# Kernel tuning notes

Measured on AMD Instinct MI355X. Metric: run time of the kernel, lower is better.

The kernel has to match this reference:

```python
import jax, jax.numpy as jnp
import numpy as np

SHIFT, REDUCE = 0, 1
B, T, E, H, V, O = 128, 256, 300, 256, 32000, 5


def _rand_trans(rng, n_tok):
    # valid shift-reduce sequence: n_tok SHIFTs, n_tok-1 REDUCEs
    seq = np.empty(2 * n_tok - 1, np.int32)
    shifts = 0
    depth = 0
    for i in range(2 * n_tok - 1):
        if shifts < n_tok and (depth < 2 or rng.random() < 0.6):
            seq[i] = SHIFT; shifts += 1; depth += 1
        else:
            seq[i] = REDUCE; depth -= 1
    return seq


def setup_inputs() -> dict:
    key = jax.random.key(0)
    ks = jax.random.split(key, 10)
    rng = np.random.default_rng(0)
    x_ids = jax.random.randint(ks[0], (B, T), 0, V)
    transitions = jnp.asarray(np.stack([_rand_trans(rng, T) for _ in range(B)], axis=1))  # [2T-1, B]
    u = lambda k, shape, s: jax.random.uniform(k, shape, jnp.float32, -s, s)
    sE = 1.0 / np.sqrt(E)
    sH = 1.0 / np.sqrt(H)
    embed_table = (jax.random.normal(ks[1], (V, E), jnp.float32) * 0.1).at[1].set(0.0)  # padding_idx=1
    return dict(
        x_ids=x_ids, transitions=transitions, embed_table=embed_table,
        Wp=u(ks[2], (H, E), sE), bp=u(ks[3], (H,), sE),
        Wg=u(ks[4], (H, E), sE), bg=u(ks[5], (H,), sE),
        Wr=u(ks[6], (5 * H, 2 * H), sH), br=u(ks[7], (5 * H,), sH),
        Wo=u(ks[8], (O, H), sH), bo=u(ks[9], (O,), sH),
    )


def reference(x_ids, transitions, embed_table, Wp, bp, Wg, bg, Wr, br, Wo, bo):
    Hh = Wp.shape[0]
    Bn, Tn = x_ids.shape
    emb = embed_table[x_ids]                                   # [B,T,E]
    c_buf = jnp.einsum('bte,he->bth', emb, Wp) + bp            # proj_x
    h_buf = jnp.tanh(c_buf) * jax.nn.sigmoid(jnp.einsum('bte,he->bth', emb, Wg) + bg)
    buffers = jnp.concatenate([h_buf, c_buf], axis=-1)         # [B,T,2H]
    bidx = jnp.arange(Bn)

    def cell(left, right):
        hl, cl = jnp.split(left, 2, axis=-1)
        hr, cr = jnp.split(right, 2, axis=-1)
        proj = jnp.concatenate([hl, hr], axis=-1) @ Wr.T + br  # [B,5H]
        i, fl, fr, g, o = jnp.split(proj, 5, axis=-1)
        c_new = jax.nn.sigmoid(i) * jnp.tanh(g) + jax.nn.sigmoid(fl) * cl + jax.nn.sigmoid(fr) * cr
        h_new = jax.nn.sigmoid(o) * jnp.tanh(c_new)
        return jnp.concatenate([h_new, c_new], axis=-1)

    def step(carry, t_batch):
        stack, sptr, bptr = carry
        is_shift = (t_batch == SHIFT)
        shifted = buffers[bidx, bptr - 1]                      # buffer.pop() = last token first
        left = stack[bidx, sptr - 2]
        right = stack[bidx, sptr - 1]
        reduced = cell(left, right)
        new_state = jnp.where(is_shift[:, None], shifted, reduced)
        new_sptr = jnp.where(is_shift, sptr + 1, sptr - 1)
        new_bptr = jnp.where(is_shift, bptr - 1, bptr)
        stack = stack.at[bidx, new_sptr - 1].set(new_state)    # push (shift or reduce result)
        return (stack, new_sptr, new_bptr), None

    init = (jnp.zeros((Bn, Tn, 2 * Hh), buffers.dtype),
            jnp.zeros((Bn,), jnp.int32), jnp.full((Bn,), Tn, jnp.int32))
    (stack, sptr, _), _ = jax.lax.scan(step, init, transitions)
    final_h = stack[bidx, sptr - 1][:, :Hh]                    # root h
    logits = final_h @ Wo.T + bo                               # dropout is identity in eval
    return logits
```

## Files before the change

### kernel.cpp

```cpp
#include <hip/hip_runtime.h>
#include <hip/hip_bf16.h>

#define B 128
#define T 256
#define E 300
#define HH 256
#define O 5
#define NSTEP (2*T - 1)
#define NINT 255
#define NG 8
#define PSTR 41
#define LMAX_DIRECT 176
#define BAR_STRIDE 16
#define BAR_WORDS ((32 + 2) * BAR_STRIDE)

__device__ __forceinline__ float sigm(float x) { return 1.f / (1.f + __expf(-x)); }

__device__ __forceinline__ void grid_barrier(unsigned* bar, int myN) {
  __syncthreads();
  if (threadIdx.x == 0) {
    __threadfence();
    const int per_sub = (int)(gridDim.x >> 5);
    const int s = (int)(blockIdx.x & 31);
    unsigned r = atomicAdd(&bar[s * BAR_STRIDE], 1u);
    if (r == (unsigned)(myN * per_sub - 1)) {
      unsigned q = atomicAdd(&bar[32 * BAR_STRIDE], 1u);
      if (q == (unsigned)(myN * 32 - 1)) {
        atomicAdd(&bar[33 * BAR_STRIDE], 1u);
      }
    }
    while (__hip_atomic_load(&bar[33 * BAR_STRIDE], __ATOMIC_ACQUIRE,
                             __HIP_MEMORY_SCOPE_AGENT) < (unsigned)myN) {
      __builtin_amdgcn_s_sleep(2);
    }
    __threadfence();
  }
  __syncthreads();
}

__global__ __launch_bounds__(256) void k_transpose(
    const float* __restrict__ Wp, const float* __restrict__ Wg,
    const float* __restrict__ Wr, float* __restrict__ WcT,
    float* __restrict__ W4) {
  int idx = blockIdx.x * 256 + threadIdx.x;
  if (idx < HH * E) {
    int h = idx / E;
    int e = idx % E;
    WcT[e * 512 + h]       = Wp[idx];
    WcT[e * 512 + 256 + h] = Wg[idx];
  }
  if (idx < 5 * HH * 2 * HH) {
    int j = idx / 512;
    int k = idx % 512;
    W4[((size_t)(k >> 2) * 1280 + j) * 4 + (k & 3)] = Wr[idx];
  }
}

#define TT 16
__global__ __launch_bounds__(256) void k_buffers(
    const int* __restrict__ x_ids, const float* __restrict__ embed,
    const float* __restrict__ WcT, const float* __restrict__ bp,
    const float* __restrict__ bg, float* __restrict__ buffers) {
  __shared__ float lds[TT * E];
  const int b  = blockIdx.y;
  const int t0 = blockIdx.x * TT;
  const int tid = threadIdx.x;

  for (int i = tid; i < TT * E; i += 256) {
    int t = i / E;
    int e = i % E;
    int id = x_ids[b * T + t0 + t];
    lds[i] = embed[(size_t)id * E + e];
  }
  __syncthreads();

  const int h = tid;
  float accP[TT], accG[TT];
#pragma unroll
  for (int t = 0; t < TT; ++t) { accP[t] = bp[h]; accG[t] = bg[h]; }

  for (int e = 0; e < E; ++e) {
    float wp = WcT[e * 512 + h];
    float wg = WcT[e * 512 + 256 + h];
#pragma unroll
    for (int t = 0; t < TT; ++t) {
      float x = lds[t * E + e];
      accP[t] = fmaf(x, wp, accP[t]);
      accG[t] = fmaf(x, wg, accG[t]);
    }
  }

#pragma unroll
  for (int t = 0; t < TT; ++t) {
    float c  = accP[t];
    float hb = tanhf(c) * sigm(accG[t]);
    size_t base = ((size_t)b * T + t0 + t) * 512;
    buffers[base + h]       = hb;
    buffers[base + 256 + h] = c;
  }
}

__global__ __launch_bounds__(128) void k_prep(
    const int* __restrict__ trans, int* __restrict__ meta,
    int* __restrict__ levCnt, int* __restrict__ levOff, int* __restrict__ maxLevG,
    int* __restrict__ rootA, unsigned* __restrict__ worklist,
    unsigned short* __restrict__ stkG, unsigned* __restrict__ bar) {
  __shared__ int cnt[256];
  __shared__ int off[256];
  __shared__ int cur[256];
  const int b = threadIdx.x;
  for (int i = b; i < 256; i += 128) cnt[i] = 0;
  for (int i = b; i < BAR_WORDS; i += 128) bar[i] = 0u;
  __syncthreads();

  int sp = 0, bp = T, r = 0;
  for (int s = 0; s < NSTEP; ++s) {
    int tr = trans[s * B + b];
    if (tr == 0) {
      stkG[sp * 128 + b] = (unsigned short)(bp - 1);
      sp++; bp--;
    } else {
      int idR = stkG[(sp - 1) * 128 + b];
      int idL = stkG[(sp - 2) * 128 + b];
      sp -= 2;
      int lL = (idL < 256) ? 0 : (meta[b * NINT + idL - 256] >> 18);
      int lR = (idR < 256) ? 0 : (meta[b * NINT + idR - 256] >> 18);
      int lev = max(lL, lR) + 1;
      meta[b * NINT + r] = idL | (idR << 9) | (lev << 18);
      atomicAdd(&cnt[lev], 1);
      stkG[sp * 128 + b] = (unsigned short)(256 + r);
      sp++; r++;
    }
  }
  rootA[b] = (int)stkG[0 * 128 + b];
  __syncthreads();

  if (b == 0) {
    int acc = 0, ml = 1;
    for (int l = 0; l < 256; ++l) {
      off[l] = acc; acc += cnt[l];
      if (cnt[l] > 0) ml = l;
    }
    *maxLevG = ml;
  }
  __syncthreads();
  for (int i = b; i < 256; i += 128) { levCnt[i] = cnt[i]; levOff[i] = off[i]; cur[i] = off[i]; }
  __syncthreads();

  for (int i = 0; i < NINT; ++i) {
    int lev = meta[b * NINT + i] >> 18;
    int pos = atomicAdd(&cur[lev], 1);
    worklist[pos] = (unsigned)((b << 9) | (256 + i));
  }
}

__device__ __forceinline__ void do_level(
    int cnt, int woff,
    const float* __restrict__ W4, const float* __restrict__ br,
    const int* __restrict__ meta, const unsigned* __restrict__ worklist,
    const float* __restrict__ buffers, float* __restrict__ internal,
    float* smem) {
  float* xs = smem;
  float* part = smem;
  const int tid  = threadIdx.x;
  const int hcol = tid & 63;
  const int kq   = tid >> 6;

  const int ngrp = (cnt + NG - 1) / NG;
  const int items = ngrp << 2;

  for (int item = blockIdx.x; item < items; item += gridDim.x) {
    const int grp = item >> 2;
    const int h0  = (item & 3) << 6;
    __syncthreads();

    const float* xlp[NG];
    const float* xrp[NG];
    float* dstp[NG];
#pragma unroll
    for (int n = 0; n < NG; ++n) {
      int wi = woff + grp * NG + n;
      if (wi >= woff + cnt) wi = woff + cnt - 1;
      unsigned w = worklist[wi];
      int node = __builtin_amdgcn_readfirstlane((int)(w & 511u));
      int bb   = __builtin_amdgcn_readfirstlane((int)(w >> 9));
      int m    = __builtin_amdgcn_readfirstlane(meta[bb * NINT + node - 256]);
      int il = m & 511, ir = (m >> 9) & 511;
      xlp[n] = (il < 256) ? (buffers + (((size_t)bb * T + il) << 9))
                          : (internal + (((size_t)bb * NINT + il - 256) << 9));
      xrp[n] = (ir < 256) ? (buffers + (((size_t)bb * T + ir) << 9))
                          : (internal + (((size_t)bb * NINT + ir - 256) << 9));
      dstp[n] = internal + (((size_t)bb * NINT + node - 256) << 9);
    }

#pragma unroll
    for (int n = 0; n < NG; ++n) {
      xs[n * 512 + tid]       = xlp[n][tid];
      xs[n * 512 + 256 + tid] = xrp[n][tid];
    }
    __syncthreads();

    float acc[5][NG];
#pragma unroll
    for (int g = 0; g < 5; ++g)
#pragma unroll
      for (int n = 0; n < NG; ++n) acc[g][n] = 0.f;

    const float4* W4v = (const float4*)W4;
    const int jb = h0 + hcol;
    const int kend = (kq << 7) + 128;
    for (int k0 = kq << 7; k0 < kend; k0 += 4) {
      const size_t kb4 = (size_t)(k0 >> 2) * 1280 + jb;
      float4 wq0 = W4v[kb4];
      float4 wq1 = W4v[kb4 + 256];
      float4 wq2 = W4v[kb4 + 512];
      float4 wq3 = W4v[kb4 + 768];
      float4 wq4 = W4v[kb4 + 1024];
      float4 xv[NG];
#pragma unroll
      for (int n = 0; n < NG; ++n)
        xv[n] = *(const float4*)&xs[n * 512 + k0];
#pragma unroll
      for (int n = 0; n < NG; ++n) {
        float s0 = acc[0][n], s1 = acc[1][n], s2 = acc[2][n], s3 = acc[3][n], s4 = acc[4][n];
        s0 = fmaf(wq0.x, xv[n].x, s0); s0 = fmaf(wq0.y, xv[n].y, s0);
        s0 = fmaf(wq0.z, xv[n].z, s0); s0 = fmaf(wq0.w, xv[n].w, s0);
        s1 = fmaf(wq1.x, xv[n].x, s1); s1 = fmaf(wq1.y, xv[n].y, s1);
        s1 = fmaf(wq1.z, xv[n].z, s1); s1 = fmaf(wq1.w, xv[n].w, s1);
        s2 = fmaf(wq2.x, xv[n].x, s2); s2 = fmaf(wq2.y, xv[n].y, s2);
        s2 = fmaf(wq2.z, xv[n].z, s2); s2 = fmaf(wq2.w, xv[n].w, s2);
        s3 = fmaf(wq3.x, xv[n].x, s3); s3 = fmaf(wq3.y, xv[n].y, s3);
        s3 = fmaf(wq3.z, xv[n].z, s3); s3 = fmaf(wq3.w, xv[n].w, s3);
        s4 = fmaf(wq4.x, xv[n].x, s4); s4 = fmaf(wq4.y, xv[n].y, s4);
        s4 = fmaf(wq4.z, xv[n].w == xv[n].w ? xv[n].w : xv[n].w, s4);
        acc[0][n] = s0; acc[1][n] = s1; acc[2][n] = s2; acc[3][n] = s3; acc[4][n] = s4;
      }
    }
    __syncthreads();

    if (kq >= 1) {
      float* pp = part + (kq - 1) * (64 * PSTR) + hcol * PSTR;
#pragma unroll
      for (int g = 0; g < 5; ++g)
#pragma unroll
        for (int n = 0; n < NG; ++n) pp[g * NG + n] = acc[g][n];
    }
    __syncthreads();

    if (kq == 0) {
      const int habs = h0 + hcol;
#pragma unroll
      for (int n = 0; n < NG; ++n) {
        float p[5];
#pragma unroll
        for (int g = 0; g < 5; ++g) {
          int pi = hcol * PSTR + g * NG + n;
          p[g] = acc[g][n]
               + part[0 * (64 * PSTR) + pi]
               + part[1 * (64 * PSTR) + pi]
               + part[2 * (64 * PSTR) + pi]
               + br[g * 256 + habs];
        }
        float cl = xlp[n][256 + habs];
        float cr = xrp[n][256 + habs];
        float ci  = sigm(p[0]);
        float cfl = sigm(p[1]);
        float cfr = sigm(p[2]);
        float tg  = tanhf(p[3]);
        float co  = sigm(p[4]);
        float cn  = ci * tg + cfl * cl + cfr * cr;
        float hn  = co * tanhf(cn);
        dstp[n][habs]       = hn;
        dstp[n][256 + habs] = cn;
      }
    }
  }
}

__global__ __launch_bounds__(256, 2) void k_level(
    int lev, const float* __restrict__ W4, const float* __restrict__ br,
    const int* __restrict__ meta, const int* __restrict__ levCnt,
    const int* __restrict__ levOff, const int* __restrict__ maxLevG,
    const unsigned* __restrict__ worklist,
    const float* __restrict__ buffers, float* __restrict__ internal) {
  __shared__ float smem[3 * 64 * PSTR];
  if (lev > *maxLevG) return;
  const int cnt = levCnt[lev];
  if (cnt == 0) return;
  do_level(cnt, levOff[lev], W4, br, meta, worklist, buffers, internal, smem);
}

__global__ __launch_bounds__(256, 2) void k_catchall(
    const float* __restrict__ W4, const float* __restrict__ br,
    const int* __restrict__ meta, const int* __restrict__ levCnt,
    const int* __restrict__ levOff, const int* __restrict__ maxLevG,
    const unsigned* __restrict__ worklist,
    const float* __restrict__ buffers, float* __restrict__ internal,
    unsigned* __restrict__ bar) {
  __shared__ float smem[3 * 64 * PSTR];
  const int maxLev = *maxLevG;
  if (maxLev <= LMAX_DIRECT) return;
  for (int lev = LMAX_DIRECT + 1; lev <= maxLev; ++lev) {
    do_level(levCnt[lev], levOff[lev], W4, br, meta, worklist, buffers, internal, smem);
    grid_barrier(bar, lev - LMAX_DIRECT);
  }
}

__global__ __launch_bounds__(256) void k_out(
    const float* __restrict__ Wo, const float* __restrict__ bo,
    const int* __restrict__ rootA, const float* __restrict__ buffers,
    const float* __restrict__ internal, float* __restrict__ out) {
  const int b = blockIdx.x;
  const int tid = threadIdx.x;
  __shared__ float red[256];
  int rid = rootA[b];
  const float* hsrc = (rid < 256) ? (buffers + (((size_t)b * T + rid) << 9))
                                  : (internal + (((size_t)b * NINT + rid - 256) << 9));
  float hj = hsrc[tid];
  for (int m = 0; m < O; ++m) {
    red[tid] = Wo[m * HH + tid] * hj;
    __syncthreads();
    for (int off = 128; off > 0; off >>= 1) {
      if (tid < off) red[tid] += red[tid + off];
      __syncthreads();
    }
    if (tid == 0) out[b * O + m] = red[0] + bo[m];
    __syncthreads();
  }
}

extern "C" void kernel_launch(void* const* d_in, const int* in_sizes, int n_in,
                              void* d_out, int out_size, void* d_ws, size_t ws_size,
                              hipStream_t stream) {
  const int*   x_ids = (const int*)d_in[0];
  const int*   trans = (const int*)d_in[1];
  const float* embed = (const float*)d_in[2];
  const float* Wp    = (const float*)d_in[3];
  const float* bp    = (const float*)d_in[4];
  const float* Wg    = (const float*)d_in[5];
  const float* bg    = (const float*)d_in[6];
  const float* Wr    = (const float*)d_in[7];
  const float* br    = (const float*)d_in[8];
  const float* Wo    = (const float*)d_in[9];
  const float* bo    = (const float*)d_in[10];
  float* out = (float*)d_out;

  float* ws       = (float*)d_ws;
  float* WcT      = ws;
  float* W4       = WcT + 300 * 512;
  float* buffers  = W4 + 512 * 1280;
  float* internal = buffers + (size_t)B * T * 512;
  int*   meta     = (int*)(internal + (size_t)B * NINT * 512);
  int*   levCnt   = meta + B * NINT;
  int*   levOff   = levCnt + 256;
  int*   maxLevG  = levOff + 256;
  int*   rootA    = maxLevG + 1;
  unsigned* worklist = (unsigned*)(rootA + B);
  unsigned short* stkG = (unsigned short*)(worklist + B * NINT);
  unsigned* bar   = (unsigned*)(stkG + 128 * 256);

  k_transpose<<<(5 * HH * 2 * HH + 255) / 256, 256, 0, stream>>>(Wp, Wg, Wr, WcT, W4);
  k_buffers<<<dim3(T / TT, B), 256, 0, stream>>>(x_ids, embed, WcT, bp, bg, buffers);
  k_prep<<<1, 128, 0, stream>>>(trans, meta, levCnt, levOff, maxLevG, rootA, worklist,
                                stkG, bar);

  for (int lev = 1; lev <= LMAX_DIRECT; ++lev) {
    int g = (lev <= 16) ? 512 : (lev <= 48) ? 256 : 128;
    k_level<<<g, 256, 0, stream>>>(lev, W4, br, meta, levCnt, levOff, maxLevG,
                                   worklist, buffers, internal);
  }

  {
    void* args[] = {(void*)&W4, (void*)&br, (void*)&meta, (void*)&levCnt, (void*)&levOff,
                    (void*)&maxLevG, (void*)&worklist, (void*)&buffers, (void*)&internal,
                    (void*)&bar};
    hipLaunchCooperativeKernel((void*)k_catchall, dim3(512), dim3(256), args, 0, stream);
  }

  k_out<<<B, 256, 0, stream>>>(Wo, bo, rootA, buffers, internal, out);
}
```

Baseline: 3.844 ms.

## Batch 16 nodes per tile, move prep parsing into LDS, unify state buffers

Doubles the number of tree nodes per work item (NG 8→16) so each loaded weight float4 is reused across more nodes, and shrinks grid sizes for the per-level launches to match. The single-block prep kernel now keeps the parse stack and node levels in LDS and stages transitions in chunks, replacing dependent global loads. Leaf and internal states are merged into one buffer addressed by 32-bit offsets. It also corrects the fifth gate's z-component FMA, which previously used the wrong input lane. The costs are more accumulator registers and a large dynamic LDS allocation for prep.

```diff
diff --git a/kernel.cpp b/kernel.cpp
--- a/kernel.cpp
+++ b/kernel.cpp
@@ -8,9 +8,11 @@
 #define O 5
 #define NSTEP (2*T - 1)
 #define NINT 255
-#define NG 8
-#define PSTR 41
+#define NG 16
+#define PSTR 81
+#define IOFF 16777216u
 #define LMAX_DIRECT 176
+#define CHUNK 96
 #define BAR_STRIDE 16
 #define BAR_WORDS ((32 + 2) * BAR_STRIDE)
 
@@ -104,7 +106,11 @@
     const int* __restrict__ trans, int* __restrict__ meta,
     int* __restrict__ levCnt, int* __restrict__ levOff, int* __restrict__ maxLevG,
     int* __restrict__ rootA, unsigned* __restrict__ worklist,
-    unsigned short* __restrict__ stkG, unsigned* __restrict__ bar) {
+    unsigned* __restrict__ bar) {
+  extern __shared__ char dynls[];
+  unsigned short* stkL = (unsigned short*)dynls;
+  unsigned char*  levL = (unsigned char*)(dynls + 65536);
+  int*            tch  = (int*)(dynls + 65536 + 32640);
   __shared__ int cnt[256];
   __shared__ int off[256];
   __shared__ int cur[256];
@@ -114,25 +120,32 @@
   __syncthreads();
 
   int sp = 0, bp = T, r = 0;
-  for (int s = 0; s < NSTEP; ++s) {
-    int tr = trans[s * B + b];
-    if (tr == 0) {
-      stkG[sp * 128 + b] = (unsigned short)(bp - 1);
-      sp++; bp--;
-    } else {
-      int idR = stkG[(sp - 1) * 128 + b];
-      int idL = stkG[(sp - 2) * 128 + b];
-      sp -= 2;
-      int lL = (idL < 256) ? 0 : (meta[b * NINT + idL - 256] >> 18);
-      int lR = (idR < 256) ? 0 : (meta[b * NINT + idR - 256] >> 18);
-      int lev = max(lL, lR) + 1;
-      meta[b * NINT + r] = idL | (idR << 9) | (lev << 18);
-      atomicAdd(&cnt[lev], 1);
-      stkG[sp * 128 + b] = (unsigned short)(256 + r);
-      sp++; r++;
-    }
-  }
-  rootA[b] = (int)stkG[0 * 128 + b];
+  for (int c0 = 0; c0 < NSTEP; c0 += CHUNK) {
+    const int cend = min(NSTEP - c0, CHUNK);
+    __syncthreads();
+    for (int i = b; i < cend * 128; i += 128) tch[i] = trans[c0 * 128 + i];
+    __syncthreads();
+    for (int s = 0; s < cend; ++s) {
+      int tr = tch[s * 128 + b];
+      if (tr == 0) {
+        stkL[sp * 128 + b] = (unsigned short)(bp - 1);
+        sp++; bp--;
+      } else {
+        int idR = stkL[(sp - 1) * 128 + b];
+        int idL = stkL[(sp - 2) * 128 + b];
+        sp -= 2;
+        int lL = (idL < 256) ? 0 : (int)levL[(idL - 256) * 128 + b];
+        int lR = (idR < 256) ? 0 : (int)levL[(idR - 256) * 128 + b];
+        int lev = max(lL, lR) + 1;
+        levL[r * 128 + b] = (unsigned char)lev;
+        meta[b * NINT + r] = idL | (idR << 9) | (lev << 18);
+        atomicAdd(&cnt[lev], 1);
+        stkL[sp * 128 + b] = (unsigned short)(256 + r);
+        sp++; r++;
+      }
+    }
+  }
+  rootA[b] = (int)stkL[0 * 128 + b];
   __syncthreads();
 
   if (b == 0) {
@@ -148,7 +161,7 @@
   __syncthreads();
 
   for (int i = 0; i < NINT; ++i) {
-    int lev = meta[b * NINT + i] >> 18;
+    int lev = (int)levL[i * 128 + b];
     int pos = atomicAdd(&cur[lev], 1);
     worklist[pos] = (unsigned)((b << 9) | (256 + i));
   }
@@ -158,10 +171,7 @@
     int cnt, int woff,
     const float* __restrict__ W4, const float* __restrict__ br,
     const int* __restrict__ meta, const unsigned* __restrict__ worklist,
-    const float* __restrict__ buffers, float* __restrict__ internal,
-    float* smem) {
-  float* xs = smem;
-  float* part = smem;
+    float* __restrict__ states, float* smem) {
   const int tid  = threadIdx.x;
   const int hcol = tid & 63;
   const int kq   = tid >> 6;
@@ -174,9 +184,7 @@
     const int h0  = (item & 3) << 6;
     __syncthreads();
 
-    const float* xlp[NG];
-    const float* xrp[NG];
-    float* dstp[NG];
+    unsigned offL[NG], offR[NG], offD[NG];
 #pragma unroll
     for (int n = 0; n < NG; ++n) {
       int wi = woff + grp * NG + n;
@@ -186,92 +194,95 @@
       int bb   = __builtin_amdgcn_readfirstlane((int)(w >> 9));
       int m    = __builtin_amdgcn_readfirstlane(meta[bb * NINT + node - 256]);
       int il = m & 511, ir = (m >> 9) & 511;
-      xlp[n] = (il < 256) ? (buffers + (((size_t)bb * T + il) << 9))
-                          : (internal + (((size_t)bb * NINT + il - 256) << 9));
-      xrp[n] = (ir < 256) ? (buffers + (((size_t)bb * T + ir) << 9))
-                          : (internal + (((size_t)bb * NINT + ir - 256) << 9));
-      dstp[n] = internal + (((size_t)bb * NINT + node - 256) << 9);
-    }
-
+      offL[n] = (il < 256) ? ((unsigned)(bb * T + il) << 9)
+                           : (IOFF + ((unsigned)(bb * NINT + il - 256) << 9));
+      offR[n] = (ir < 256) ? ((unsigned)(bb * T + ir) << 9)
+                           : (IOFF + ((unsigned)(bb * NINT + ir - 256) << 9));
+      offD[n] = IOFF + ((unsigned)(bb * NINT + node - 256) << 9);
+    }
+
+    float* xs = smem;
 #pragma unroll
     for (int n = 0; n < NG; ++n) {
-      xs[n * 512 + tid]       = xlp[n][tid];
-      xs[n * 512 + 256 + tid] = xrp[n][tid];
-    }
-    __syncthreads();
-
-    float acc[5][NG];
-#pragma unroll
-    for (int g = 0; g < 5; ++g)
-#pragma unroll
-      for (int n = 0; n < NG; ++n) acc[g][n] = 0.f;
+      xs[n * 512 + tid]       = states[(size_t)offL[n] + tid];
+      xs[n * 512 + 256 + tid] = states[(size_t)offR[n] + tid];
+    }
+    __syncthreads();
+
+    float a0[NG], a1[NG], a2[NG], a3[NG], a4[NG];
+#pragma unroll
+    for (int n = 0; n < NG; ++n) { a0[n]=0.f; a1[n]=0.f; a2[n]=0.f; a3[n]=0.f; a4[n]=0.f; }
 
     const float4* W4v = (const float4*)W4;
     const int jb = h0 + hcol;
-    const int kend = (kq << 7) + 128;
-    for (int k0 = kq << 7; k0 < kend; k0 += 4) {
-      const size_t kb4 = (size_t)(k0 >> 2) * 1280 + jb;
-      float4 wq0 = W4v[kb4];
-      float4 wq1 = W4v[kb4 + 256];
-      float4 wq2 = W4v[kb4 + 512];
-      float4 wq3 = W4v[kb4 + 768];
-      float4 wq4 = W4v[kb4 + 1024];
-      float4 xv[NG];
-#pragma unroll
-      for (int n = 0; n < NG; ++n)
-        xv[n] = *(const float4*)&xs[n * 512 + k0];
+    const int k4end = (kq << 5) + 32;
+    for (int k4 = kq << 5; k4 < k4end; ++k4) {
+      const size_t kb4 = (size_t)k4 * 1280 + jb;
+      float4 w0 = W4v[kb4];
+      float4 w1 = W4v[kb4 + 256];
+      float4 w2 = W4v[kb4 + 512];
+      float4 w3 = W4v[kb4 + 768];
+      float4 w4 = W4v[kb4 + 1024];
 #pragma unroll
       for (int n = 0; n < NG; ++n) {
-        float s0 = acc[0][n], s1 = acc[1][n], s2 = acc[2][n], s3 = acc[3][n], s4 = acc[4][n];
-        s0 = fmaf(wq0.x, xv[n].x, s0); s0 = fmaf(wq0.y, xv[n].y, s0);
-        s0 = fmaf(wq0.z, xv[n].z, s0); s0 = fmaf(wq0.w, xv[n].w, s0);
-        s1 = fmaf(wq1.x, xv[n].x, s1); s1 = fmaf(wq1.y, xv[n].y, s1);
-        s1 = fmaf(wq1.z, xv[n].z, s1); s1 = fmaf(wq1.w, xv[n].w, s1);
-        s2 = fmaf(wq2.x, xv[n].x, s2); s2 = fmaf(wq2.y, xv[n].y, s2);
-        s2 = fmaf(wq2.z, xv[n].z, s2); s2 = fmaf(wq2.w, xv[n].w, s2);
-        s3 = fmaf(wq3.x, xv[n].x, s3); s3 = fmaf(wq3.y, xv[n].y, s3);
-        s3 = fmaf(wq3.z, xv[n].z, s3); s3 = fmaf(wq3.w, xv[n].w, s3);
-        s4 = fmaf(wq4.x, xv[n].x, s4); s4 = fmaf(wq4.y, xv[n].y, s4);
-        s4 = fmaf(wq4.z, xv[n].w == xv[n].w ? xv[n].w : xv[n].w, s4);
-        acc[0][n] = s0; acc[1][n] = s1; acc[2][n] = s2; acc[3][n] = s3; acc[4][n] = s4;
+        float4 xv = *(const float4*)&xs[n * 512 + (k4 << 2)];
+        float s0 = a0[n], s1 = a1[n], s2 = a2[n], s3 = a3[n], s4 = a4[n];
+        s0 = fmaf(w0.x, xv.x, s0); s0 = fmaf(w0.y, xv.y, s0);
+        s0 = fmaf(w0.z, xv.z, s0); s0 = fmaf(w0.w, xv.w, s0);
+        s1 = fmaf(w1.x, xv.x, s1); s1 = fmaf(w1.y, xv.y, s1);
+        s1 = fmaf(w1.z, xv.z, s1); s1 = fmaf(w1.w, xv.w, s1);
+        s2 = fmaf(w2.x, xv.x, s2); s2 = fmaf(w2.y, xv.y, s2);
+        s2 = fmaf(w2.z, xv.z, s2); s2 = fmaf(w2.w, xv.w, s2);
+        s3 = fmaf(w3.x, xv.x, s3); s3 = fmaf(w3.y, xv.y, s3);
+        s3 = fmaf(w3.z, xv.z, s3); s3 = fmaf(w3.w, xv.w, s3);
+        s4 = fmaf(w4.x, xv.x, s4); s4 = fmaf(w4.y, xv.y, s4);
+        s4 = fmaf(w4.z, xv.z, s4); s4 = fmaf(w4.w, xv.w, s4);
+        a0[n] = s0; a1[n] = s1; a2[n] = s2; a3[n] = s3; a4[n] = s4;
       }
     }
     __syncthreads();
 
     if (kq >= 1) {
-      float* pp = part + (kq - 1) * (64 * PSTR) + hcol * PSTR;
-#pragma unroll
-      for (int g = 0; g < 5; ++g)
-#pragma unroll
-        for (int n = 0; n < NG; ++n) pp[g * NG + n] = acc[g][n];
+      float* pp = smem + (kq - 1) * (64 * PSTR) + hcol * PSTR;
+#pragma unroll
+      for (int n = 0; n < NG; ++n) {
+        pp[n]          = a0[n];
+        pp[NG + n]     = a1[n];
+        pp[2 * NG + n] = a2[n];
+        pp[3 * NG + n] = a3[n];
+        pp[4 * NG + n] = a4[n];
+      }
     }
     __syncthreads();
 
     if (kq == 0) {
       const int habs = h0 + hcol;
+      const float b0 = br[habs];
+      const float b1 = br[256 + habs];
+      const float b2 = br[512 + habs];
+      const float b3 = br[768 + habs];
+      const float b4 = br[1024 + habs];
 #pragma unroll
       for (int n = 0; n < NG; ++n) {
-        float p[5];
-#pragma unroll
-        for (int g = 0; g < 5; ++g) {
-          int pi = hcol * PSTR + g * NG + n;
-          p[g] = acc[g][n]
-               + part[0 * (64 * PSTR) + pi]
-               + part[1 * (64 * PSTR) + pi]
-               + part[2 * (64 * PSTR) + pi]
-               + br[g * 256 + habs];
-        }
-        float cl = xlp[n][256 + habs];
-        float cr = xrp[n][256 + habs];
-        float ci  = sigm(p[0]);
-        float cfl = sigm(p[1]);
-        float cfr = sigm(p[2]);
-        float tg  = tanhf(p[3]);
-        float co  = sigm(p[4]);
+        const float* q0 = smem + 0 * (64 * PSTR) + hcol * PSTR;
+        const float* q1 = smem + 1 * (64 * PSTR) + hcol * PSTR;
+        const float* q2 = smem + 2 * (64 * PSTR) + hcol * PSTR;
+        float p0 = a0[n] + q0[n]          + q1[n]          + q2[n]          + b0;
+        float p1 = a1[n] + q0[NG + n]     + q1[NG + n]     + q2[NG + n]     + b1;
+        float p2 = a2[n] + q0[2 * NG + n] + q1[2 * NG + n] + q2[2 * NG + n] + b2;
+        float p3 = a3[n] + q0[3 * NG + n] + q1[3 * NG + n] + q2[3 * NG + n] + b3;
+        float p4 = a4[n] + q0[4 * NG + n] + q1[4 * NG + n] + q2[4 * NG + n] + b4;
+        float cl = states[(size_t)offL[n] + 256 + habs];
+        float cr = states[(size_t)offR[n] + 256 + habs];
+        float ci  = sigm(p0);
+        float cfl = sigm(p1);
+        float cfr = sigm(p2);
+        float tg  = tanhf(p3);
+        float co  = sigm(p4);
         float cn  = ci * tg + cfl * cl + cfr * cr;
         float hn  = co * tanhf(cn);
-        dstp[n][habs]       = hn;
-        dstp[n][256 + habs] = cn;
+        states[(size_t)offD[n] + habs]       = hn;
+        states[(size_t)offD[n] + 256 + habs] = cn;
       }
     }
   }
@@ -281,42 +292,40 @@
     int lev, const float* __restrict__ W4, const float* __restrict__ br,
     const int* __restrict__ meta, const int* __restrict__ levCnt,
     const int* __restrict__ levOff, const int* __restrict__ maxLevG,
-    const unsigned* __restrict__ worklist,
-    const float* __restrict__ buffers, float* __restrict__ internal) {
+    const unsigned* __restrict__ worklist, float* __restrict__ states) {
   __shared__ float smem[3 * 64 * PSTR];
   if (lev > *maxLevG) return;
   const int cnt = levCnt[lev];
   if (cnt == 0) return;
-  do_level(cnt, levOff[lev], W4, br, meta, worklist, buffers, internal, smem);
+  do_level(cnt, levOff[lev], W4, br, meta, worklist, states, smem);
 }
 
 __global__ __launch_bounds__(256, 2) void k_catchall(
     const float* __restrict__ W4, const float* __restrict__ br,
     const int* __restrict__ meta, const int* __restrict__ levCnt,
     const int* __restrict__ levOff, const int* __restrict__ maxLevG,
-    const unsigned* __restrict__ worklist,
-    const float* __restrict__ buffers, float* __restrict__ internal,
+    const unsigned* __restrict__ worklist, float* __restrict__ states,
     unsigned* __restrict__ bar) {
   __shared__ float smem[3 * 64 * PSTR];
   const int maxLev = *maxLevG;
   if (maxLev <= LMAX_DIRECT) return;
   for (int lev = LMAX_DIRECT + 1; lev <= maxLev; ++lev) {
-    do_level(levCnt[lev], levOff[lev], W4, br, meta, worklist, buffers, internal, smem);
+    do_level(levCnt[lev], levOff[lev], W4, br, meta, worklist, states, smem);
     grid_barrier(bar, lev - LMAX_DIRECT);
   }
 }
 
 __global__ __launch_bounds__(256) void k_out(
     const float* __restrict__ Wo, const float* __restrict__ bo,
-    const int* __restrict__ rootA, const float* __restrict__ buffers,
-    const float* __restrict__ internal, float* __restrict__ out) {
+    const int* __restrict__ rootA, const float* __restrict__ states,
+    float* __restrict__ out) {
   const int b = blockIdx.x;
   const int tid = threadIdx.x;
   __shared__ float red[256];
   int rid = rootA[b];
-  const float* hsrc = (rid < 256) ? (buffers + (((size_t)b * T + rid) << 9))
-                                  : (internal + (((size_t)b * NINT + rid - 256) << 9));
-  float hj = hsrc[tid];
+  unsigned hoff = (rid < 256) ? ((unsigned)(b * T + rid) << 9)
+                              : (IOFF + ((unsigned)(b * NINT + rid - 256) << 9));
+  float hj = states[(size_t)hoff + tid];
   for (int m = 0; m < O; ++m) {
     red[tid] = Wo[m * HH + tid] * hj;
     __syncthreads();
@@ -348,34 +357,33 @@
   float* ws       = (float*)d_ws;
   float* WcT      = ws;
   float* W4       = WcT + 300 * 512;
-  float* buffers  = W4 + 512 * 1280;
-  float* internal = buffers + (size_t)B * T * 512;
-  int*   meta     = (int*)(internal + (size_t)B * NINT * 512);
+  float* states   = W4 + 512 * 1280;
+  int*   meta     = (int*)(states + (size_t)IOFF + (size_t)B * NINT * 512);
   int*   levCnt   = meta + B * NINT;
   int*   levOff   = levCnt + 256;
   int*   maxLevG  = levOff + 256;
   int*   rootA    = maxLevG + 1;
   unsigned* worklist = (unsigned*)(rootA + B);
-  unsigned short* stkG = (unsigned short*)(worklist + B * NINT);
-  unsigned* bar   = (unsigned*)(stkG + 128 * 256);
+  unsigned* bar   = worklist + B * NINT;
 
   k_transpose<<<(5 * HH * 2 * HH + 255) / 256, 256, 0, stream>>>(Wp, Wg, Wr, WcT, W4);
-  k_buffers<<<dim3(T / TT, B), 256, 0, stream>>>(x_ids, embed, WcT, bp, bg, buffers);
-  k_prep<<<1, 128, 0, stream>>>(trans, meta, levCnt, levOff, maxLevG, rootA, worklist,
-                                stkG, bar);
+  k_buffers<<<dim3(T / TT, B), 256, 0, stream>>>(x_ids, embed, WcT, bp, bg, states);
+
+  const size_t prep_lds = 65536 + 32640 + (size_t)CHUNK * 128 * 4;
+  k_prep<<<1, 128, prep_lds, stream>>>(trans, meta, levCnt, levOff, maxLevG, rootA,
+                                       worklist, bar);
 
   for (int lev = 1; lev <= LMAX_DIRECT; ++lev) {
-    int g = (lev <= 16) ? 512 : (lev <= 48) ? 256 : 128;
+    int g = (lev <= 8) ? 512 : (lev <= 24) ? 256 : (lev <= 48) ? 128 : 64;
     k_level<<<g, 256, 0, stream>>>(lev, W4, br, meta, levCnt, levOff, maxLevG,
-                                   worklist, buffers, internal);
+                                   worklist, states);
   }
 
   {
     void* args[] = {(void*)&W4, (void*)&br, (void*)&meta, (void*)&levCnt, (void*)&levOff,
-                    (void*)&maxLevG, (void*)&worklist, (void*)&buffers, (void*)&internal,
-                    (void*)&bar};
+                    (void*)&maxLevG, (void*)&worklist, (void*)&states, (void*)&bar};
     hipLaunchCooperativeKernel((void*)k_catchall, dim3(512), dim3(256), args, 0, stream);
   }
 
-  k_out<<<B, 256, 0, stream>>>(Wo, bo, rootA, buffers, internal, out);
-}
+  k_out<<<B, 256, 0, stream>>>(Wo, bo, rootA, states, out);
+}
```

New measurement: 6.012 ms. 1.56x slower.
